# Performance work log

Measured on AMD Instinct MI355X. Metric: run time of the kernel, lower is better.

The kernel has to match this reference:

```python
import jax, jax.numpy as jnp
import numpy as np

LN_EPS = 1e-5
SA_EPS = 1e-8
NUM_ITERS = 3

def layer_norm(x, w, b):
    mu = jnp.mean(x, axis=-1, keepdims=True)
    var = jnp.mean((x - mu) ** 2, axis=-1, keepdims=True)
    return (x - mu) / jnp.sqrt(var + LN_EPS) * w + b


def setup_inputs() -> dict:
    key = jax.random.key(0)
    ks = jax.random.split(key, 24)
    B, C, H, W = 128, 256, 32, 32
    D, S, MH, NC = 64, 8, 128, 15
    s = lambda k, shape, scale=0.02: jax.random.normal(k, shape, dtype=jnp.float32) * scale
    inp = {
        "x1": jax.random.normal(ks[0], (B, C, H, W), dtype=jnp.float32),
        "x2": jax.random.normal(ks[1], (B, C, H, W), dtype=jnp.float32),
        # 1x1 convs stored as [out,in]
        "conv1_w": s(ks[2], (D, C)), "conv1_b": jnp.zeros((D,), jnp.float32),
        "conv2_w": s(ks[3], (D, C)), "conv2_b": jnp.zeros((D,), jnp.float32),
        "norm_w": jnp.ones((D,), jnp.float32), "norm_b": jnp.zeros((D,), jnp.float32),
        "ni_w": jnp.ones((D,), jnp.float32), "ni_b": jnp.zeros((D,), jnp.float32),
        "ns_w": jnp.ones((D,), jnp.float32), "ns_b": jnp.zeros((D,), jnp.float32),
        "nm_w": jnp.ones((D,), jnp.float32), "nm_b": jnp.zeros((D,), jnp.float32),
        "slots_mu": s(ks[4], (1, 1, D), 1.0), "slots_log_sigma": s(ks[5], (1, 1, D), 0.1),
        "Wq": s(ks[6], (D, D), 0.1), "Wk": s(ks[7], (D, D), 0.1), "Wv": s(ks[8], (D, D), 0.1),
        "gru_wih": s(ks[9], (3 * D, D), 0.1), "gru_whh": s(ks[10], (3 * D, D), 0.1),
        "gru_bih": jnp.zeros((3 * D,), jnp.float32), "gru_bhh": jnp.zeros((3 * D,), jnp.float32),
        "mlp_w1": s(ks[11], (MH, D), 0.1), "mlp_b1": jnp.zeros((MH,), jnp.float32),
        "mlp_w2": s(ks[12], (D, MH), 0.1), "mlp_b2": jnp.zeros((D,), jnp.float32),
        "head_w": s(ks[13], (NC, D), 0.1), "head_b": jnp.zeros((NC,), jnp.float32),
        "noise": jax.random.normal(ks[14], (B, S, D), dtype=jnp.float32),
    }
    return inp


def _forward(x1, x2, conv1_w, conv1_b, conv2_w, conv2_b, norm_w, norm_b,
             ni_w, ni_b, ns_w, ns_b, nm_w, nm_b, slots_mu, slots_log_sigma,
             Wq, Wk, Wv, gru_wih, gru_whh, gru_bih, gru_bhh,
             mlp_w1, mlp_b1, mlp_w2, mlp_b2, head_w, head_b, noise):
    B = x1.shape[0]
    D = Wq.shape[0]
    # 1x1 convs then flatten to tokens: [B, H*W, D]
    t1 = jnp.einsum('bchw,dc->bhwd', x1, conv1_w).reshape(B, -1, D) + conv1_b
    t2 = jnp.einsum('bchw,dc->bhwd', x2, conv2_w).reshape(B, -1, D) + conv2_b
    inputs = jnp.concatenate([t1, t2], axis=1)          # [B, N, D]
    inputs = layer_norm(inputs, norm_w, norm_b)

    # SlotAttention
    inputs = layer_norm(inputs, ni_w, ni_b)
    k = inputs @ Wk.T                                    # [B, N, D]
    v = inputs @ Wv.T
    slots = slots_mu + jnp.exp(slots_log_sigma) * noise  # [B, S, D]
    scale = D ** -0.5
    for _ in range(NUM_ITERS):
        slots_prev = slots
        sn = layer_norm(slots, ns_w, ns_b)
        q = (sn @ Wq.T) * scale                          # [B, S, D]
        attn_logits = jnp.einsum('bnd,bsd->bns', k, q)   # [B, N, S]
        attn = jax.nn.softmax(attn_logits, axis=-1) + SA_EPS
        attn = attn / jnp.sum(attn, axis=-2, keepdims=True)
        updates = jnp.einsum('bns,bnd->bsd', attn, v)    # [B, S, D]
        # GRUCell (torch gate order: r, z, n)
        gi = updates @ gru_wih.T + gru_bih               # [B, S, 3D]
        gh = slots_prev @ gru_whh.T + gru_bhh
        ir, iz, inn = jnp.split(gi, 3, axis=-1)
        hr, hz, hn = jnp.split(gh, 3, axis=-1)
        r = jax.nn.sigmoid(ir + hr)
        z = jax.nn.sigmoid(iz + hz)
        n = jnp.tanh(inn + r * hn)
        slots = (1.0 - z) * n + z * slots_prev
        # residual MLP
        h = layer_norm(slots, nm_w, nm_b)
        h = jax.nn.relu(h @ mlp_w1.T + mlp_b1) @ mlp_w2.T + mlp_b2
        slots = slots + h

    fused = jnp.mean(slots, axis=1)                      # [B, D]
    return fused @ head_w.T + head_b                     # [B, n_classes]


def reference(x1, x2, conv1_w, conv1_b, conv2_w, conv2_b, norm_w, norm_b,
              ni_w, ni_b, ns_w, ns_b, nm_w, nm_b, slots_mu, slots_log_sigma,
              Wq, Wk, Wv, gru_wih, gru_whh, gru_bih, gru_bhh,
              mlp_w1, mlp_b1, mlp_w2, mlp_b2, head_w, head_b, noise):
    return _forward(x1, x2, conv1_w, conv1_b, conv2_w, conv2_b, norm_w, norm_b,
                    ni_w, ni_b, ns_w, ns_b, nm_w, nm_b, slots_mu, slots_log_sigma,
                    Wq, Wk, Wv, gru_wih, gru_whh, gru_bih, gru_bhh,
                    mlp_w1, mlp_b1, mlp_w2, mlp_b2, head_w, head_b, noise)
```

## Files before the change

### kernel.cpp

```cpp
#include <hip/hip_runtime.h>
#include <stdint.h>


typedef __bf16 bf16;
typedef __bf16 bf16x8 __attribute__((ext_vector_type(8)));
typedef float  f32x4  __attribute__((ext_vector_type(4)));

#define MFMA16(a, b, c) __builtin_amdgcn_mfma_f32_16x16x32_bf16((a), (b), (c), 0, 0, 0)

#define ASYNC_LDS16(g, l) \
  __builtin_amdgcn_global_load_lds((const __attribute__((address_space(1))) void*)(g), \
                                   (__attribute__((address_space(3))) void*)(l), 16, 0, 0)

__global__ __launch_bounds__(256) void k0_convert(
    const float* __restrict__ c1w, const float* __restrict__ c2w,
    const float* __restrict__ wk,  const float* __restrict__ wvv,
    bf16* __restrict__ wconv, bf16* __restrict__ wkv)
{
  const int i = blockIdx.x * 256 + threadIdx.x;
  if (i < 16384) {
    wconv[i]         = (bf16)c1w[i];
    wconv[16384 + i] = (bf16)c2w[i];
  }
  if (i < 4096) {
    wkv[i]        = (bf16)wk[i];
    wkv[4096 + i] = (bf16)wvv[i];
  }
}

__global__ __launch_bounds__(256) void k1_conv_kv(
    const float* __restrict__ x1, const float* __restrict__ x2,
    const float* __restrict__ c1b, const float* __restrict__ c2b,
    const float* __restrict__ nw,  const float* __restrict__ nb,
    const float* __restrict__ niw, const float* __restrict__ nib,
    const bf16* __restrict__ wconv, const bf16* __restrict__ wkv,
    bf16* __restrict__ kbuf, bf16* __restrict__ vT)
{
  __shared__ union {
    float xs[32 * 264];
    struct { float T[64][65]; bf16 tok[64][72]; } p2;
    struct { float Tk[64][65]; float Tv[64][65]; } kv;
  } U;

  const int bx   = blockIdx.x;
  const int tile = bx & 15;
  const int img  = (bx >> 4) & 1;
  const int b    = bx >> 5;
  const int tid  = threadIdx.x;
  const int lane = tid & 63;
  const int wvid = tid >> 6;
  const int l15  = lane & 15;
  const int quad = lane >> 4;

  const float* xp  = (img ? x2 : x1) + (size_t)b * (256 * 1024) + tile * 64;
  const int   rowin = lane >> 4;
  const int   pq    = (lane & 15) * 4;
  const float* ga0  = xp + (size_t)rowin * 1024 + pq;
  const bf16* wc = wconv + img * (64 * 256);
  const int p = wvid * 16 + l15;

  f32x4 acc[4] = {{0.f,0.f,0.f,0.f},{0.f,0.f,0.f,0.f},{0.f,0.f,0.f,0.f},{0.f,0.f,0.f,0.f}};

  for (int half = 0; half < 2; ++half) {
    #pragma unroll
    for (int gi = 0; gi < 8; ++gi) {
      const int g = wvid + gi * 4;
      ASYNC_LDS16(ga0 + (size_t)(half * 128 + g * 4) * 1024, &U.xs[g * 264]);
    }
    __syncthreads();
    #pragma unroll
    for (int k0 = 0; k0 < 128; k0 += 32) {
      bf16x8 af;
      #pragma unroll
      for (int j = 0; j < 8; ++j) {
        const int c = k0 + quad * 8 + j;
        af[j] = (bf16)U.xs[(c >> 2) * 264 + (c & 3) * 64 + p];
      }
      #pragma unroll
      for (int nt = 0; nt < 4; ++nt) {
        const bf16x8 bw = *(const bf16x8*)&wc[(nt * 16 + l15) * 256 + half * 128 + k0 + quad * 8];
        acc[nt] = MFMA16(af, bw, acc[nt]);
      }
    }
    __syncthreads();
  }

  {
    const float* cb = img ? c2b : c1b;
    #pragma unroll
    for (int nt = 0; nt < 4; ++nt) {
      const int d = nt * 16 + l15;
      const float bias = cb[d];
      #pragma unroll
      for (int r = 0; r < 4; ++r)
        U.p2.T[wvid * 16 + quad * 4 + r][d] = acc[nt][r] + bias;
    }
  }
  __syncthreads();

  {
    const int pix = tid >> 2, part = tid & 3;
    float xv[16], yv[16];
    float s = 0.f, s2 = 0.f;
    #pragma unroll
    for (int i = 0; i < 16; ++i) {
      xv[i] = U.p2.T[pix][part * 16 + i];
      s += xv[i]; s2 += xv[i] * xv[i];
    }
    s  += __shfl_xor(s, 1);  s  += __shfl_xor(s, 2);
    s2 += __shfl_xor(s2, 1); s2 += __shfl_xor(s2, 2);
    float mu   = s * 0.015625f;
    float rstd = rsqrtf(s2 * 0.015625f - mu * mu + 1e-5f);
    s = 0.f; s2 = 0.f;
    #pragma unroll
    for (int i = 0; i < 16; ++i) {
      const int d = part * 16 + i;
      const float y = (xv[i] - mu) * rstd * nw[d] + nb[d];
      yv[i] = y; s += y; s2 += y * y;
    }
    s  += __shfl_xor(s, 1);  s  += __shfl_xor(s, 2);
    s2 += __shfl_xor(s2, 1); s2 += __shfl_xor(s2, 2);
    mu   = s * 0.015625f;
    rstd = rsqrtf(s2 * 0.015625f - mu * mu + 1e-5f);
    #pragma unroll
    for (int i = 0; i < 16; ++i) {
      const int d = part * 16 + i;
      U.p2.tok[pix][d] = (bf16)((yv[i] - mu) * rstd * niw[d] + nib[d]);
    }
  }
  __syncthreads();

  f32x4 ak[4] = {{0.f,0.f,0.f,0.f},{0.f,0.f,0.f,0.f},{0.f,0.f,0.f,0.f},{0.f,0.f,0.f,0.f}};
  f32x4 av[4] = {{0.f,0.f,0.f,0.f},{0.f,0.f,0.f,0.f},{0.f,0.f,0.f,0.f},{0.f,0.f,0.f,0.f}};
  #pragma unroll
  for (int k0 = 0; k0 < 64; k0 += 32) {
    const bf16x8 af = *(const bf16x8*)&U.p2.tok[wvid * 16 + l15][k0 + quad * 8];
    #pragma unroll
    for (int nt = 0; nt < 4; ++nt) {
      const bf16x8 bk = *(const bf16x8*)&wkv[(nt * 16 + l15) * 64 + k0 + quad * 8];
      const bf16x8 bv = *(const bf16x8*)&wkv[4096 + (nt * 16 + l15) * 64 + k0 + quad * 8];
      ak[nt] = MFMA16(af, bk, ak[nt]);
      av[nt] = MFMA16(af, bv, av[nt]);
    }
  }
  __syncthreads();

  #pragma unroll
  for (int nt = 0; nt < 4; ++nt)
    #pragma unroll
    for (int r = 0; r < 4; ++r) {
      U.kv.Tk[wvid * 16 + quad * 4 + r][nt * 16 + l15] = ak[nt][r];
      U.kv.Tv[nt * 16 + l15][wvid * 16 + quad * 4 + r] = av[nt][r];
    }
  __syncthreads();
  {
    const int row = tid >> 2, dd = (tid & 3) * 16;
    const size_t kb = ((size_t)b * 2048 + img * 1024 + tile * 64) * 64;
    bf16 tb[16];
    #pragma unroll
    for (int i = 0; i < 16; ++i) tb[i] = (bf16)U.kv.Tk[row][dd + i];
    *(bf16x8*)&kbuf[kb + (size_t)row * 64 + dd]     = *(bf16x8*)&tb[0];
    *(bf16x8*)&kbuf[kb + (size_t)row * 64 + dd + 8] = *(bf16x8*)&tb[8];
    #pragma unroll
    for (int i = 0; i < 16; ++i) tb[i] = (bf16)U.kv.Tv[row][dd + i];
    const size_t vb = ((size_t)b * 64 + row) * 2048 + img * 1024 + tile * 64 + dd;
    *(bf16x8*)&vT[vb]     = *(bf16x8*)&tb[0];
    *(bf16x8*)&vT[vb + 8] = *(bf16x8*)&tb[8];
  }
}

__global__ __launch_bounds__(512) void kS0(
    const float* __restrict__ smu, const float* __restrict__ slog,
    const float* __restrict__ noise,
    const float* __restrict__ nsw, const float* __restrict__ nsb,
    const float* __restrict__ Wq,
    float* __restrict__ slotbuf, bf16* __restrict__ qbuf)
{
  __shared__ float tmp[8][66];
  const int b = blockIdx.x, tid = threadIdx.x;
  const int s0 = tid >> 6, d0 = tid & 63;
  const int part = tid & 7, sl = (tid >> 3) & 7, wv = tid >> 6;

  const float sval = smu[d0] + expf(slog[d0]) * noise[((size_t)b * 8 + s0) * 64 + d0];
  slotbuf[((size_t)b * 8 + s0) * 64 + d0] = sval;
  float s = sval, s2 = sval * sval;
  #pragma unroll
  for (int m = 1; m < 64; m <<= 1) { s += __shfl_xor(s, m); s2 += __shfl_xor(s2, m); }
  const float mu = s * 0.015625f;
  const float rstd = rsqrtf(s2 * 0.015625f - mu * mu + 1e-5f);
  tmp[s0][d0] = (sval - mu) * rstd * nsw[d0] + nsb[d0];
  __syncthreads();

  float tm[8];
  #pragma unroll
  for (int i = 0; i < 8; ++i) tm[i] = tmp[sl][part * 8 + i];
  for (int orr = 0; orr < 8; ++orr) {
    const int d = orr * 8 + wv;
    const f32x4 w0 = *(const f32x4*)&Wq[d * 64 + part * 8];
    const f32x4 w1v = *(const f32x4*)&Wq[d * 64 + part * 8 + 4];
    float a = tm[0]*w0[0] + tm[1]*w0[1] + tm[2]*w0[2] + tm[3]*w0[3]
            + tm[4]*w1v[0] + tm[5]*w1v[1] + tm[6]*w1v[2] + tm[7]*w1v[3];
    a += __shfl_xor(a, 1); a += __shfl_xor(a, 2); a += __shfl_xor(a, 4);
    if (part == 0) qbuf[((size_t)b * 8 + sl) * 64 + d] = (bf16)(a * 0.125f);
  }
}

__global__ __launch_bounds__(256) void kA(
    const bf16* __restrict__ kbuf, const bf16* __restrict__ vT,
    const bf16* __restrict__ qbuf,
    float* __restrict__ updpart, float* __restrict__ colpart)
{
  __shared__ bf16  qs[16][72];
  __shared__ bf16  attn_b[16][136];
  __shared__ float updp[4][8][64];
  __shared__ float cspart[4][8];

  const int bx  = blockIdx.x;
  const int b   = bx >> 4, ch = bx & 15;
  const int tid = threadIdx.x;
  const int lane = tid & 63, wvid = tid >> 6;
  const int l15 = lane & 15, quad = lane >> 4;
  const size_t tokbase = (size_t)b * 2048 + ch * 128;

  if (tid < 64) {
    const int s = tid >> 3, o = (tid & 7) * 8;
    *(bf16x8*)&qs[s][o] = *(const bf16x8*)&qbuf[((size_t)b * 8 + s) * 64 + o];
  } else if (tid < 128) {
    const int s = 8 + ((tid - 64) >> 3), o = ((tid - 64) & 7) * 8;
    uint32_t* zp = (uint32_t*)&qs[s][o];
    zp[0] = 0u; zp[1] = 0u; zp[2] = 0u; zp[3] = 0u;
  }
  {
    uint32_t* az = (uint32_t*)&attn_b[8][0];
    for (int i = tid; i < 544; i += 256) az[i] = 0u;
  }
  __syncthreads();

  {
    float cs = 0.f;
    #pragma unroll
    for (int mt = 0; mt < 2; ++mt) {
      const int t0 = wvid * 32 + mt * 16;
      const bf16* kr = kbuf + (tokbase + t0 + l15) * 64 + quad * 8;
      f32x4 lg = {0.f, 0.f, 0.f, 0.f};
      lg = MFMA16(*(const bf16x8*)&kr[0],  *(const bf16x8*)&qs[l15][quad * 8],      lg);
      lg = MFMA16(*(const bf16x8*)&kr[32], *(const bf16x8*)&qs[l15][32 + quad * 8], lg);
      #pragma unroll
      for (int r = 0; r < 4; ++r) {
        const float l = lg[r];
        float m = l;
        m = fmaxf(m, __shfl_xor(m, 1));
        m = fmaxf(m, __shfl_xor(m, 2));
        m = fmaxf(m, __shfl_xor(m, 4));
        const float e = expf(l - m);
        float ss = e;
        ss += __shfl_xor(ss, 1);
        ss += __shfl_xor(ss, 2);
        ss += __shfl_xor(ss, 4);
        const float at = e / ss + 1e-8f;
        if (l15 < 8) {
          const bf16 ab = (bf16)at;
          attn_b[l15][t0 + quad * 4 + r] = ab;
          cs += (float)ab;
        }
      }
    }
    cs += __shfl_xor(cs, 16);
    cs += __shfl_xor(cs, 32);
    if (lane < 8) cspart[wvid][lane] = cs;
  }
  __syncthreads();

  {
    const bf16x8 afr = *(const bf16x8*)&attn_b[l15][wvid * 32 + quad * 8];
    const bf16* vrow = vT + (size_t)b * 131072 + (size_t)ch * 128 + wvid * 32 + quad * 8;
    const f32x4 zero4 = {0.f, 0.f, 0.f, 0.f};
    #pragma unroll
    for (int nt = 0; nt < 4; ++nt) {
      const bf16x8 bv = *(const bf16x8*)&vrow[(size_t)(nt * 16 + l15) * 2048];
      f32x4 dd = MFMA16(afr, bv, zero4);
      if (quad < 2) {
        #pragma unroll
        for (int r = 0; r < 4; ++r)
          updp[wvid][quad * 4 + r][nt * 16 + l15] = dd[r];
      }
    }
  }
  __syncthreads();

  {
    const float* up = &updp[0][0][0];
    float* og = updpart + ((size_t)b * 16 + ch) * 512;
    for (int o = tid; o < 512; o += 256)
      og[o] = up[o] + up[o + 512] + up[o + 1024] + up[o + 1536];
    if (tid < 8)
      colpart[((size_t)b * 16 + ch) * 8 + tid] =
        cspart[0][tid] + cspart[1][tid] + cspart[2][tid] + cspart[3][tid];
  }
}

__global__ __launch_bounds__(512) void kB(
    const float* __restrict__ updpart, const float* __restrict__ colpart,
    float* __restrict__ slotbuf, bf16* __restrict__ qbuf,
    const float* __restrict__ nsw, const float* __restrict__ nsb,
    const float* __restrict__ nmw, const float* __restrict__ nmb,
    const float* __restrict__ Wq,
    const float* __restrict__ wih, const float* __restrict__ whh,
    const float* __restrict__ bih, const float* __restrict__ bhh,
    const float* __restrict__ w1,  const float* __restrict__ b1,
    const float* __restrict__ w2,  const float* __restrict__ b2,
    const float* __restrict__ hwt, const float* __restrict__ hb,
    float* __restrict__ out, const int last)
{
  __shared__ float slots[8][66];
  __shared__ float tmp[8][66];
  __shared__ float gig[8][192], ghg[8][192];
  __shared__ float h1[8][132];
  const int b = blockIdx.x, tid = threadIdx.x;
  const int s0 = tid >> 6, d0 = tid & 63;
  const int part = tid & 7, sl = (tid >> 3) & 7, wv = tid >> 6;

  {
    const float* up = updpart + (size_t)b * 8192 + s0 * 64 + d0;
    float u = 0.f;
    #pragma unroll
    for (int ch = 0; ch < 16; ++ch) u += up[ch * 512];
    const float* cp = colpart + (size_t)b * 128 + s0;
    float cs = 0.f;
    #pragma unroll
    for (int ch = 0; ch < 16; ++ch) cs += cp[ch * 8];
    tmp[s0][d0] = u / cs;
    slots[s0][d0] = slotbuf[((size_t)b * 8 + s0) * 64 + d0];
  }
  __syncthreads();

  {
    float tv[8], sv[8];
    #pragma unroll
    for (int i = 0; i < 8; ++i) { tv[i] = tmp[sl][part * 8 + i]; sv[i] = slots[sl][part * 8 + i]; }
    for (int jr = 0; jr < 24; ++jr) {
      const int j = jr * 8 + wv;
      const f32x4 wa0 = *(const f32x4*)&wih[j * 64 + part * 8];
      const f32x4 wa1 = *(const f32x4*)&wih[j * 64 + part * 8 + 4];
      const f32x4 wb0 = *(const f32x4*)&whh[j * 64 + part * 8];
      const f32x4 wb1 = *(const f32x4*)&whh[j * 64 + part * 8 + 4];
      float a = tv[0]*wa0[0] + tv[1]*wa0[1] + tv[2]*wa0[2] + tv[3]*wa0[3]
              + tv[4]*wa1[0] + tv[5]*wa1[1] + tv[6]*wa1[2] + tv[7]*wa1[3];
      float h = sv[0]*wb0[0] + sv[1]*wb0[1] + sv[2]*wb0[2] + sv[3]*wb0[3]
              + sv[4]*wb1[0] + sv[5]*wb1[1] + sv[6]*wb1[2] + sv[7]*wb1[3];
      a += __shfl_xor(a, 1); a += __shfl_xor(a, 2); a += __shfl_xor(a, 4);
      h += __shfl_xor(h, 1); h += __shfl_xor(h, 2); h += __shfl_xor(h, 4);
      if (part == 0) { gig[sl][j] = a + bih[j]; ghg[sl][j] = h + bhh[j]; }
    }
  }
  __syncthreads();

  float snew;
  {
    const float r  = 1.f / (1.f + expf(-(gig[s0][d0]       + ghg[s0][d0])));
    const float z  = 1.f / (1.f + expf(-(gig[s0][64 + d0]  + ghg[s0][64 + d0])));
    const float nn = tanhf(gig[s0][128 + d0] + r * ghg[s0][128 + d0]);
    snew = (1.f - z) * nn + z * slots[s0][d0];
    slots[s0][d0] = snew;
  }
  {
    float s = snew, s2 = snew * snew;
    #pragma unroll
    for (int m = 1; m < 64; m <<= 1) { s += __shfl_xor(s, m); s2 += __shfl_xor(s2, m); }
    const float mu = s * 0.015625f;
    const float rstd = rsqrtf(s2 * 0.015625f - mu * mu + 1e-5f);
    tmp[s0][d0] = (snew - mu) * rstd * nmw[d0] + nmb[d0];
  }
  __syncthreads();

  {
    float tm[8];
    #pragma unroll
    for (int i = 0; i < 8; ++i) tm[i] = tmp[sl][part * 8 + i];
    for (int jr = 0; jr < 16; ++jr) {
      const int j = jr * 8 + wv;
      const f32x4 w0 = *(const f32x4*)&w1[j * 64 + part * 8];
      const f32x4 w1v = *(const f32x4*)&w1[j * 64 + part * 8 + 4];
      float a = tm[0]*w0[0] + tm[1]*w0[1] + tm[2]*w0[2] + tm[3]*w0[3]
              + tm[4]*w1v[0] + tm[5]*w1v[1] + tm[6]*w1v[2] + tm[7]*w1v[3];
      a += __shfl_xor(a, 1); a += __shfl_xor(a, 2); a += __shfl_xor(a, 4);
      if (part == 0) h1[sl][j] = fmaxf(a + b1[j], 0.f);
    }
  }
  __syncthreads();

  for (int orr = 0; orr < 8; ++orr) {
    const int d = orr * 8 + wv;
    float a = 0.f;
    #pragma unroll
    for (int i = 0; i < 4; ++i) {
      const f32x4 wv4 = *(const f32x4*)&w2[d * 128 + part * 16 + i * 4];
      a += h1[sl][part * 16 + i * 4 + 0] * wv4[0] + h1[sl][part * 16 + i * 4 + 1] * wv4[1]
         + h1[sl][part * 16 + i * 4 + 2] * wv4[2] + h1[sl][part * 16 + i * 4 + 3] * wv4[3];
    }
    a += __shfl_xor(a, 1); a += __shfl_xor(a, 2); a += __shfl_xor(a, 4);
    if (part == 0) slots[sl][d] += a + b2[d];
  }
  __syncthreads();

  const float sfin = slots[s0][d0];
  slotbuf[((size_t)b * 8 + s0) * 64 + d0] = sfin;

  if (!last) {
    float s = sfin, s2 = sfin * sfin;
    #pragma unroll
    for (int m = 1; m < 64; m <<= 1) { s += __shfl_xor(s, m); s2 += __shfl_xor(s2, m); }
    const float mu = s * 0.015625f;
    const float rstd = rsqrtf(s2 * 0.015625f - mu * mu + 1e-5f);
    tmp[s0][d0] = (sfin - mu) * rstd * nsw[d0] + nsb[d0];
    __syncthreads();
    float tm[8];
    #pragma unroll
    for (int i = 0; i < 8; ++i) tm[i] = tmp[sl][part * 8 + i];
    for (int orr = 0; orr < 8; ++orr) {
      const int d = orr * 8 + wv;
      const f32x4 w0 = *(const f32x4*)&Wq[d * 64 + part * 8];
      const f32x4 w1v = *(const f32x4*)&Wq[d * 64 + part * 8 + 4];
      float a = tm[0]*w0[0] + tm[1]*w0[1] + tm[2]*w0[2] + tm[3]*w0[3]
              + tm[4]*w1v[0] + tm[5]*w1v[1] + tm[6]*w1v[2] + tm[7]*w1v[3];
      a += __shfl_xor(a, 1); a += __shfl_xor(a, 2); a += __shfl_xor(a, 4);
      if (part == 0) qbuf[((size_t)b * 8 + sl) * 64 + d] = (bf16)(a * 0.125f);
    }
  } else {
    if (tid < 64) {
      float f = 0.f;
      #pragma unroll
      for (int s = 0; s < 8; ++s) f += slots[s][tid];
      tmp[0][tid] = f * 0.125f;
    }
    __syncthreads();
    if (tid < 15) {
      float a = hb[tid];
      for (int d = 0; d < 64; ++d) a += tmp[0][d] * hwt[tid * 64 + d];
      out[b * 15 + tid] = a;
    }
  }
}

extern "C" void kernel_launch(void* const* d_in, const int* in_sizes, int n_in,
                              void* d_out, int out_size, void* d_ws, size_t ws_size,
                              hipStream_t stream) {
  const float* x1   = (const float*)d_in[0];
  const float* x2   = (const float*)d_in[1];
  const float* c1w  = (const float*)d_in[2];
  const float* c1b  = (const float*)d_in[3];
  const float* c2w  = (const float*)d_in[4];
  const float* c2b  = (const float*)d_in[5];
  const float* nw   = (const float*)d_in[6];
  const float* nb   = (const float*)d_in[7];
  const float* niw  = (const float*)d_in[8];
  const float* nib  = (const float*)d_in[9];
  const float* nsw  = (const float*)d_in[10];
  const float* nsb  = (const float*)d_in[11];
  const float* nmw  = (const float*)d_in[12];
  const float* nmb  = (const float*)d_in[13];
  const float* smu  = (const float*)d_in[14];
  const float* slog = (const float*)d_in[15];
  const float* Wq   = (const float*)d_in[16];
  const float* Wk   = (const float*)d_in[17];
  const float* Wv   = (const float*)d_in[18];
  const float* wih  = (const float*)d_in[19];
  const float* whh  = (const float*)d_in[20];
  const float* bih  = (const float*)d_in[21];
  const float* bhh  = (const float*)d_in[22];
  const float* w1   = (const float*)d_in[23];
  const float* b1   = (const float*)d_in[24];
  const float* w2   = (const float*)d_in[25];
  const float* b2   = (const float*)d_in[26];
  const float* hwt  = (const float*)d_in[27];
  const float* hb   = (const float*)d_in[28];
  const float* noise= (const float*)d_in[29];

  char* ws = (char*)d_ws;
  bf16*  kbuf    = (bf16*)(ws);
  bf16*  vT      = (bf16*)(ws + (size_t)33554432);
  bf16*  wconv   = (bf16*)(ws + (size_t)67108864);
  bf16*  wkv     = (bf16*)(ws + (size_t)67174400);
  float* slotbuf = (float*)(ws + (size_t)67190784);
  bf16*  qbuf    = (bf16*)(ws + (size_t)67452928);
  float* updpart = (float*)(ws + (size_t)67584000);
  float* colpart = (float*)(ws + (size_t)71778304);

  k0_convert<<<dim3(64), dim3(256), 0, stream>>>(c1w, c2w, Wk, Wv, wconv, wkv);
  k1_conv_kv<<<dim3(4096), dim3(256), 0, stream>>>(x1, x2, c1b, c2b, nw, nb, niw, nib,
                                                   wconv, wkv, kbuf, vT);
  kS0<<<dim3(128), dim3(512), 0, stream>>>(smu, slog, noise, nsw, nsb, Wq, slotbuf, qbuf);
  for (int it = 0; it < 3; ++it) {
    kA<<<dim3(2048), dim3(256), 0, stream>>>(kbuf, vT, qbuf, updpart, colpart);
    kB<<<dim3(128), dim3(512), 0, stream>>>(updpart, colpart, slotbuf, qbuf,
                                            nsw, nsb, nmw, nmb, Wq,
                                            wih, whh, bih, bhh, w1, b1, w2, b2,
                                            hwt, hb, (float*)d_out, (it == 2) ? 1 : 0);
  }
}
```

Baseline: 526.4 us.

## Fuse slot-attention iterations into one cooperative persistent kernel with grid sync

Replaces the per-iteration kA/kB launches and the initial slot kernel with a single cooperative kernel. Two blocks per batch split the tokens, exchange partial updates through global memory, and meet at a grid-wide sync. Slots, queries, GRU and MLP state stay in shared memory across iterations. This removes launch overhead and global round-trips for slot state. In exchange the attention phase runs on only 256 blocks, with less parallelism and latency hiding than the previous 2048-block kernel, and it relies on cooperative launch, falling back to the old path if that fails.

```diff
diff --git a/kernel.cpp b/kernel.cpp
--- a/kernel.cpp
+++ b/kernel.cpp
@@ -1,4 +1,5 @@
 #include <hip/hip_runtime.h>
+#include <hip/hip_cooperative_groups.h>
 #include <stdint.h>
 
 
@@ -166,6 +167,246 @@
     const size_t vb = ((size_t)b * 64 + row) * 2048 + img * 1024 + tile * 64 + dd;
     *(bf16x8*)&vT[vb]     = *(bf16x8*)&tb[0];
     *(bf16x8*)&vT[vb + 8] = *(bf16x8*)&tb[8];
+  }
+}
+
+__global__ __launch_bounds__(512, 2) void kIter(
+    const bf16* __restrict__ kbuf, const bf16* __restrict__ vT,
+    const float* __restrict__ smu, const float* __restrict__ slog,
+    const float* __restrict__ noise,
+    const float* __restrict__ nsw, const float* __restrict__ nsb,
+    const float* __restrict__ nmw, const float* __restrict__ nmb,
+    const float* __restrict__ Wq,
+    const float* __restrict__ wih, const float* __restrict__ whh,
+    const float* __restrict__ bih, const float* __restrict__ bhh,
+    const float* __restrict__ w1,  const float* __restrict__ b1,
+    const float* __restrict__ w2,  const float* __restrict__ b2,
+    const float* __restrict__ hwt, const float* __restrict__ hb,
+    float* out, float* partg, float* colg)
+{
+  __shared__ float slots[8][66];
+  __shared__ float tmp[8][66];
+  __shared__ bf16  qs[16][72];
+  __shared__ bf16  attn_b[16][328];
+  __shared__ float updp[8][8][64];
+  __shared__ float cspart[8][8];
+  __shared__ float gig[8][192], ghg[8][192];
+  __shared__ float h1[8][132];
+
+  const int bx  = blockIdx.x;
+  const int b   = bx >> 1, bh = bx & 1;
+  const int tid = threadIdx.x;
+  const int lane = tid & 63, wvid = tid >> 6;
+  const int l15 = lane & 15, quad = lane >> 4;
+  const int s0 = wvid, d0 = lane;
+  const int part = tid & 7, sl = (tid >> 3) & 7;
+
+  {
+    const float sval = smu[d0] + expf(slog[d0]) * noise[((size_t)b * 8 + s0) * 64 + d0];
+    slots[s0][d0] = sval;
+    float s = sval, s2 = sval * sval;
+    #pragma unroll
+    for (int m = 1; m < 64; m <<= 1) { s += __shfl_xor(s, m); s2 += __shfl_xor(s2, m); }
+    const float mu = s * 0.015625f;
+    const float rstd = rsqrtf(s2 * 0.015625f - mu * mu + 1e-5f);
+    tmp[s0][d0] = (sval - mu) * rstd * nsw[d0] + nsb[d0];
+  }
+  for (int i = tid; i < 288;  i += 512) ((uint32_t*)&qs[8][0])[i] = 0u;
+  for (int i = tid; i < 1312; i += 512) ((uint32_t*)&attn_b[8][0])[i] = 0u;
+  __syncthreads();
+  {
+    float tm[8];
+    #pragma unroll
+    for (int i = 0; i < 8; ++i) tm[i] = tmp[sl][part * 8 + i];
+    for (int orr = 0; orr < 8; ++orr) {
+      const int d = orr * 8 + wvid;
+      const f32x4 w0 = *(const f32x4*)&Wq[d * 64 + part * 8];
+      const f32x4 w1v = *(const f32x4*)&Wq[d * 64 + part * 8 + 4];
+      float a = tm[0]*w0[0] + tm[1]*w0[1] + tm[2]*w0[2] + tm[3]*w0[3]
+              + tm[4]*w1v[0] + tm[5]*w1v[1] + tm[6]*w1v[2] + tm[7]*w1v[3];
+      a += __shfl_xor(a, 1); a += __shfl_xor(a, 2); a += __shfl_xor(a, 4);
+      if (part == 0) qs[sl][d] = (bf16)(a * 0.125f);
+    }
+  }
+  __syncthreads();
+
+  for (int it = 0; it < 3; ++it) {
+    f32x4 ua[4] = {{0.f,0.f,0.f,0.f},{0.f,0.f,0.f,0.f},{0.f,0.f,0.f,0.f},{0.f,0.f,0.f,0.f}};
+    float csacc = 0.f;
+    const size_t tokbase = (size_t)b * 2048 + bh * 1024;
+    for (int p = 0; p < 4; ++p) {
+      const int t0w = p * 256 + wvid * 32;
+      const bf16* vrow = vT + (size_t)b * 131072 + (size_t)(bh * 1024 + t0w) + quad * 8;
+      const bf16x8 bv0 = *(const bf16x8*)&vrow[(size_t)(l15)      * 2048];
+      const bf16x8 bv1 = *(const bf16x8*)&vrow[(size_t)(16 + l15) * 2048];
+      const bf16x8 bv2 = *(const bf16x8*)&vrow[(size_t)(32 + l15) * 2048];
+      const bf16x8 bv3 = *(const bf16x8*)&vrow[(size_t)(48 + l15) * 2048];
+      #pragma unroll
+      for (int mt = 0; mt < 2; ++mt) {
+        const bf16* kr = kbuf + (tokbase + t0w + mt * 16 + l15) * 64 + quad * 8;
+        f32x4 lg = {0.f, 0.f, 0.f, 0.f};
+        lg = MFMA16(*(const bf16x8*)&kr[0],  *(const bf16x8*)&qs[l15][quad * 8],      lg);
+        lg = MFMA16(*(const bf16x8*)&kr[32], *(const bf16x8*)&qs[l15][32 + quad * 8], lg);
+        #pragma unroll
+        for (int r = 0; r < 4; ++r) {
+          const float l = lg[r];
+          float m = l;
+          m = fmaxf(m, __shfl_xor(m, 1));
+          m = fmaxf(m, __shfl_xor(m, 2));
+          m = fmaxf(m, __shfl_xor(m, 4));
+          const float e = expf(l - m);
+          float ss = e;
+          ss += __shfl_xor(ss, 1);
+          ss += __shfl_xor(ss, 2);
+          ss += __shfl_xor(ss, 4);
+          const float at = e / ss + 1e-8f;
+          if (l15 < 8) {
+            const bf16 ab = (bf16)at;
+            attn_b[l15][wvid * 40 + mt * 16 + quad * 4 + r] = ab;
+            csacc += (float)ab;
+          }
+        }
+      }
+      const bf16x8 afr = *(const bf16x8*)&attn_b[l15][wvid * 40 + quad * 8];
+      ua[0] = MFMA16(afr, bv0, ua[0]);
+      ua[1] = MFMA16(afr, bv1, ua[1]);
+      ua[2] = MFMA16(afr, bv2, ua[2]);
+      ua[3] = MFMA16(afr, bv3, ua[3]);
+    }
+    if (quad < 2) {
+      #pragma unroll
+      for (int nt = 0; nt < 4; ++nt)
+        #pragma unroll
+        for (int r = 0; r < 4; ++r)
+          updp[wvid][quad * 4 + r][nt * 16 + l15] = ua[nt][r];
+    }
+    csacc += __shfl_xor(csacc, 16);
+    csacc += __shfl_xor(csacc, 32);
+    if (lane < 8) cspart[wvid][lane] = csacc;
+    __syncthreads();
+    {
+      float u = 0.f;
+      #pragma unroll
+      for (int w2i = 0; w2i < 8; ++w2i) u += updp[w2i][s0][d0];
+      partg[((size_t)(it & 1) * 256 + bx) * 512 + tid] = u;
+      if (tid < 8) {
+        float c = 0.f;
+        #pragma unroll
+        for (int w2i = 0; w2i < 8; ++w2i) c += cspart[w2i][tid];
+        colg[(size_t)(it & 1) * 2048 + bx * 8 + tid] = c;
+      }
+    }
+    cooperative_groups::this_grid().sync();
+    {
+      const float* pg0 = partg + ((size_t)(it & 1) * 256 + b * 2) * 512;
+      const float u = pg0[tid] + pg0[512 + tid];
+      const float* cg0 = colg + (size_t)(it & 1) * 2048 + b * 16;
+      tmp[s0][d0] = u / (cg0[s0] + cg0[8 + s0]);
+    }
+    __syncthreads();
+
+    {
+      float tv[8], sv[8];
+      #pragma unroll
+      for (int i = 0; i < 8; ++i) { tv[i] = tmp[sl][part * 8 + i]; sv[i] = slots[sl][part * 8 + i]; }
+      for (int jr = 0; jr < 24; ++jr) {
+        const int j = jr * 8 + wvid;
+        const f32x4 wa0 = *(const f32x4*)&wih[j * 64 + part * 8];
+        const f32x4 wa1 = *(const f32x4*)&wih[j * 64 + part * 8 + 4];
+        const f32x4 wb0 = *(const f32x4*)&whh[j * 64 + part * 8];
+        const f32x4 wb1 = *(const f32x4*)&whh[j * 64 + part * 8 + 4];
+        float a = tv[0]*wa0[0] + tv[1]*wa0[1] + tv[2]*wa0[2] + tv[3]*wa0[3]
+                + tv[4]*wa1[0] + tv[5]*wa1[1] + tv[6]*wa1[2] + tv[7]*wa1[3];
+        float hv = sv[0]*wb0[0] + sv[1]*wb0[1] + sv[2]*wb0[2] + sv[3]*wb0[3]
+                 + sv[4]*wb1[0] + sv[5]*wb1[1] + sv[6]*wb1[2] + sv[7]*wb1[3];
+        a  += __shfl_xor(a, 1);  a  += __shfl_xor(a, 2);  a  += __shfl_xor(a, 4);
+        hv += __shfl_xor(hv, 1); hv += __shfl_xor(hv, 2); hv += __shfl_xor(hv, 4);
+        if (part == 0) { gig[sl][j] = a + bih[j]; ghg[sl][j] = hv + bhh[j]; }
+      }
+    }
+    __syncthreads();
+
+    {
+      const float rr = 1.f / (1.f + expf(-(gig[s0][d0]      + ghg[s0][d0])));
+      const float z  = 1.f / (1.f + expf(-(gig[s0][64 + d0] + ghg[s0][64 + d0])));
+      const float nn = tanhf(gig[s0][128 + d0] + rr * ghg[s0][128 + d0]);
+      const float snew = (1.f - z) * nn + z * slots[s0][d0];
+      slots[s0][d0] = snew;
+      float s = snew, s2 = snew * snew;
+      #pragma unroll
+      for (int m = 1; m < 64; m <<= 1) { s += __shfl_xor(s, m); s2 += __shfl_xor(s2, m); }
+      const float mu = s * 0.015625f;
+      const float rstd = rsqrtf(s2 * 0.015625f - mu * mu + 1e-5f);
+      tmp[s0][d0] = (snew - mu) * rstd * nmw[d0] + nmb[d0];
+    }
+    __syncthreads();
+
+    {
+      float tm[8];
+      #pragma unroll
+      for (int i = 0; i < 8; ++i) tm[i] = tmp[sl][part * 8 + i];
+      for (int jr = 0; jr < 16; ++jr) {
+        const int j = jr * 8 + wvid;
+        const f32x4 w0 = *(const f32x4*)&w1[j * 64 + part * 8];
+        const f32x4 w1v = *(const f32x4*)&w1[j * 64 + part * 8 + 4];
+        float a = tm[0]*w0[0] + tm[1]*w0[1] + tm[2]*w0[2] + tm[3]*w0[3]
+                + tm[4]*w1v[0] + tm[5]*w1v[1] + tm[6]*w1v[2] + tm[7]*w1v[3];
+        a += __shfl_xor(a, 1); a += __shfl_xor(a, 2); a += __shfl_xor(a, 4);
+        if (part == 0) h1[sl][j] = fmaxf(a + b1[j], 0.f);
+      }
+    }
+    __syncthreads();
+
+    for (int orr = 0; orr < 8; ++orr) {
+      const int d = orr * 8 + wvid;
+      float a = 0.f;
+      #pragma unroll
+      for (int i = 0; i < 4; ++i) {
+        const f32x4 wv4 = *(const f32x4*)&w2[d * 128 + part * 16 + i * 4];
+        a += h1[sl][part * 16 + i * 4 + 0] * wv4[0] + h1[sl][part * 16 + i * 4 + 1] * wv4[1]
+           + h1[sl][part * 16 + i * 4 + 2] * wv4[2] + h1[sl][part * 16 + i * 4 + 3] * wv4[3];
+      }
+      a += __shfl_xor(a, 1); a += __shfl_xor(a, 2); a += __shfl_xor(a, 4);
+      if (part == 0) slots[sl][d] += a + b2[d];
+    }
+    __syncthreads();
+
+    if (it < 2) {
+      const float sfin = slots[s0][d0];
+      float s = sfin, s2 = sfin * sfin;
+      #pragma unroll
+      for (int m = 1; m < 64; m <<= 1) { s += __shfl_xor(s, m); s2 += __shfl_xor(s2, m); }
+      const float mu = s * 0.015625f;
+      const float rstd = rsqrtf(s2 * 0.015625f - mu * mu + 1e-5f);
+      tmp[s0][d0] = (sfin - mu) * rstd * nsw[d0] + nsb[d0];
+      __syncthreads();
+      float tm[8];
+      #pragma unroll
+      for (int i = 0; i < 8; ++i) tm[i] = tmp[sl][part * 8 + i];
+      for (int orr = 0; orr < 8; ++orr) {
+        const int d = orr * 8 + wvid;
+        const f32x4 w0 = *(const f32x4*)&Wq[d * 64 + part * 8];
+        const f32x4 w1v = *(const f32x4*)&Wq[d * 64 + part * 8 + 4];
+        float a = tm[0]*w0[0] + tm[1]*w0[1] + tm[2]*w0[2] + tm[3]*w0[3]
+                + tm[4]*w1v[0] + tm[5]*w1v[1] + tm[6]*w1v[2] + tm[7]*w1v[3];
+        a += __shfl_xor(a, 1); a += __shfl_xor(a, 2); a += __shfl_xor(a, 4);
+        if (part == 0) qs[sl][d] = (bf16)(a * 0.125f);
+      }
+      __syncthreads();
+    }
+  }
+
+  if (tid < 64) {
+    float f = 0.f;
+    #pragma unroll
+    for (int s = 0; s < 8; ++s) f += slots[s][tid];
+    tmp[0][tid] = f * 0.125f;
+  }
+  __syncthreads();
+  if (bh == 0 && tid < 15) {
+    float a = hb[tid];
+    for (int d = 0; d < 64; ++d) a += tmp[0][d] * hwt[tid * 64 + d];
+    out[b * 15 + tid] = a;
   }
 }
 
@@ -485,16 +726,30 @@
   bf16*  qbuf    = (bf16*)(ws + (size_t)67452928);
   float* updpart = (float*)(ws + (size_t)67584000);
   float* colpart = (float*)(ws + (size_t)71778304);
+  float* partg   = (float*)(ws + (size_t)67584000);
+  float* colg    = (float*)(ws + (size_t)68632576);
+  float* outp    = (float*)d_out;
 
   k0_convert<<<dim3(64), dim3(256), 0, stream>>>(c1w, c2w, Wk, Wv, wconv, wkv);
   k1_conv_kv<<<dim3(4096), dim3(256), 0, stream>>>(x1, x2, c1b, c2b, nw, nb, niw, nib,
                                                    wconv, wkv, kbuf, vT);
-  kS0<<<dim3(128), dim3(512), 0, stream>>>(smu, slog, noise, nsw, nsb, Wq, slotbuf, qbuf);
-  for (int it = 0; it < 3; ++it) {
-    kA<<<dim3(2048), dim3(256), 0, stream>>>(kbuf, vT, qbuf, updpart, colpart);
-    kB<<<dim3(128), dim3(512), 0, stream>>>(updpart, colpart, slotbuf, qbuf,
-                                            nsw, nsb, nmw, nmb, Wq,
-                                            wih, whh, bih, bhh, w1, b1, w2, b2,
-                                            hwt, hb, (float*)d_out, (it == 2) ? 1 : 0);
+
+  void* kargs[] = {
+    (void*)&kbuf, (void*)&vT, (void*)&smu, (void*)&slog, (void*)&noise,
+    (void*)&nsw, (void*)&nsb, (void*)&nmw, (void*)&nmb, (void*)&Wq,
+    (void*)&wih, (void*)&whh, (void*)&bih, (void*)&bhh,
+    (void*)&w1, (void*)&b1, (void*)&w2, (void*)&b2,
+    (void*)&hwt, (void*)&hb, (void*)&outp, (void*)&partg, (void*)&colg };
+  hipError_t ce = hipLaunchCooperativeKernel((const void*)kIter, dim3(256), dim3(512),
+                                             kargs, 0u, stream);
+  if (ce != hipSuccess) {
+    kS0<<<dim3(128), dim3(512), 0, stream>>>(smu, slog, noise, nsw, nsb, Wq, slotbuf, qbuf);
+    for (int itr = 0; itr < 3; ++itr) {
+      kA<<<dim3(2048), dim3(256), 0, stream>>>(kbuf, vT, qbuf, updpart, colpart);
+      kB<<<dim3(128), dim3(512), 0, stream>>>(updpart, colpart, slotbuf, qbuf,
+                                              nsw, nsb, nmw, nmb, Wq,
+                                              wih, whh, bih, bhh, w1, b1, w2, b2,
+                                              hwt, hb, outp, (itr == 2) ? 1 : 0);
+    }
   }
 }
```

After: 725.7 us. 37.9% more time.
